# Performance work log

Measured on AMD Instinct MI355X. Metric: run time of the kernel, lower is better.

## Reference

```python
import jax, jax.numpy as jnp
import numpy as np

N = 32768       # tokens
D_IN = 1024     # input_dim
D_OUT = 1024    # output_dim
E = 8           # num_experts
TOP_K = 2


def setup_inputs() -> dict:
    key = jax.random.key(0)
    k1, k2, k3, k4, k5 = jax.random.split(key, 5)
    scale = 1.0 / np.sqrt(D_IN)
    return {
        "x": jax.random.normal(k1, (N, D_IN), dtype=jnp.float32),
        "Wg": jax.random.uniform(k2, (E, D_IN), jnp.float32, -scale, scale),
        "bg": jax.random.uniform(k3, (E,), jnp.float32, -scale, scale),
        "W": jax.random.uniform(k4, (E, D_OUT, D_IN), jnp.float32, -scale, scale),
        "b": jax.random.uniform(k5, (E, D_OUT), jnp.float32, -scale, scale),
    }


def reference(x, Wg, bg, W, b):
    # Gating: softmax over experts, then top-k (weights NOT renormalized,
    # matching the original module).
    gate_scores = x @ Wg.T + bg                      # [N, E]
    gate_probs = jax.nn.softmax(gate_scores, axis=-1)
    topk_w, topk_idx = jax.lax.top_k(gate_probs, TOP_K)  # [N, K]

    # Per-token combine weight for each expert: sum_k w_k * onehot(idx_k)
    combine = (jax.nn.one_hot(topk_idx, E, dtype=x.dtype)
               * topk_w[..., None]).sum(axis=1)      # [N, E]

    # Dense per-expert GEMM + weighted combine (loop over small fixed E).
    out = jnp.zeros((x.shape[0], D_OUT), dtype=x.dtype)
    for e in range(E):
        out = out + combine[:, e:e + 1] * (x @ W[e].T + b[e])
    return out
```

## Files before the change

kernel.cpp:

```cpp
#include <hip/hip_runtime.h>
#include <hip/hip_bf16.h>
#include <cstdint>
#include <cstddef>

#define N_TOK   32768
#define D_IN    1024
#define D_OUT   1024
#define NE      8

#define BM 256
#define BN 256
#define BK 32
#define NTILES (D_IN / BK)

typedef __attribute__((ext_vector_type(4))) float floatx4;
typedef __attribute__((ext_vector_type(8))) short bf16x8;

__device__ __forceinline__ unsigned short f2bf(float f) {
  union { float f; unsigned int u; } v; v.f = f;
  unsigned int u = v.u + 0x7fffu + ((v.u >> 16) & 1u);
  return (unsigned short)(u >> 16);
}

__device__ __forceinline__ unsigned short f2h(float f) {
  union { _Float16 hf; unsigned short us; } c; c.hf = (_Float16)f; return c.us;
}
__device__ __forceinline__ float h2f(unsigned short u) {
  union { _Float16 hf; unsigned short us; } c; c.us = u; return (float)c.hf;
}

__device__ __forceinline__ void gload_lds16(const void* g, void* l) {
  __builtin_amdgcn_global_load_lds(
      (const __attribute__((address_space(1))) unsigned int*)g,
      (__attribute__((address_space(3))) unsigned int*)l, 16, 0, 0);
}

__global__ __launch_bounds__(256) void prep_kernel(
    const float* __restrict__ x,
    const float* __restrict__ Wg,
    const float* __restrict__ bg,
    const float* __restrict__ W,
    unsigned short* __restrict__ xb,
    unsigned short* __restrict__ Wb,
    int* __restrict__ counts,
    int* __restrict__ bids,
    float* __restrict__ bw,
    int* __restrict__ tok2slot,
    float* __restrict__ out,
    int zero_out)
{
  __shared__ float wg_lds[NE * D_IN];
  __shared__ int lcnt[NE];
  __shared__ int basee[NE];
  __shared__ int   tok_e[64][2];
  __shared__ int   tok_s[64][2];
  __shared__ float tok_w[64][2];

  const int blk = blockIdx.x;
  const int tid = threadIdx.x;

  if (blk >= 1024) {
    if (!zero_out) return;
    float4* o4 = (float4*)out;
    const int base = (blk - 1024) * 4096;
#pragma unroll
    for (int i = 0; i < 16; ++i)
      o4[base + i * 256 + tid] = (float4){0.f, 0.f, 0.f, 0.f};
    return;
  }
  if (blk >= 512) {
    const float4* s = (const float4*)W;
    const int base = (blk - 512) * 4096;
#pragma unroll
    for (int i = 0; i < 16; ++i) {
      int idx = base + i * 256 + tid;
      float4 v = s[idx];
      ushort4 h;
      h.x = f2bf(v.x); h.y = f2bf(v.y); h.z = f2bf(v.z); h.w = f2bf(v.w);
      ((ushort4*)Wb)[idx] = h;
    }
    return;
  }

  {
    const float4* s = (const float4*)Wg;
    float4* d = (float4*)wg_lds;
    for (int i = tid; i < NE * D_IN / 4; i += 256) d[i] = s[i];
  }
  if (tid < NE) lcnt[tid] = 0;
  __syncthreads();

  const int wave = tid >> 6, lane = tid & 63;
  const float4* x4 = (const float4*)x;
  const float4* w4 = (const float4*)wg_lds;

  for (int t = 0; t < 16; ++t) {
    const int lt = wave * 16 + t;
    const int n  = blk * 64 + lt;
    float4 xv[4];
    float acc[NE];
#pragma unroll
    for (int e = 0; e < NE; ++e) acc[e] = 0.f;
#pragma unroll
    for (int j = 0; j < 4; ++j) {
      xv[j] = x4[(size_t)n * 256 + j * 64 + lane];
#pragma unroll
      for (int e = 0; e < NE; ++e) {
        float4 w = w4[e * 256 + j * 64 + lane];
        acc[e] += xv[j].x * w.x + xv[j].y * w.y + xv[j].z * w.z + xv[j].w * w.w;
      }
    }
#pragma unroll
    for (int j = 0; j < 4; ++j) {
      ushort4 h;
      h.x = f2bf(xv[j].x); h.y = f2bf(xv[j].y);
      h.z = f2bf(xv[j].z); h.w = f2bf(xv[j].w);
      ((ushort4*)xb)[(size_t)n * 256 + j * 64 + lane] = h;
    }
#pragma unroll
    for (int e = 0; e < NE; ++e)
#pragma unroll
      for (int s = 32; s > 0; s >>= 1)
        acc[e] += __shfl_xor(acc[e], s, 64);

    if (lane == 0) {
      float sc[NE];
#pragma unroll
      for (int e = 0; e < NE; ++e) sc[e] = acc[e] + bg[e];
      float m = sc[0];
#pragma unroll
      for (int e = 1; e < NE; ++e) m = fmaxf(m, sc[e]);
      float p[NE], den = 0.f;
#pragma unroll
      for (int e = 0; e < NE; ++e) { p[e] = __expf(sc[e] - m); den += p[e]; }
      int e1 = 0;
#pragma unroll
      for (int e = 1; e < NE; ++e) if (sc[e] > sc[e1]) e1 = e;
      int e2 = (e1 == 0) ? 1 : 0;
#pragma unroll
      for (int e = 0; e < NE; ++e) if (e != e1 && sc[e] > sc[e2]) e2 = e;
      float inv = 1.f / den;
      tok_e[lt][0] = e1; tok_w[lt][0] = p[e1] * inv; tok_s[lt][0] = atomicAdd(&lcnt[e1], 1);
      tok_e[lt][1] = e2; tok_w[lt][1] = p[e2] * inv; tok_s[lt][1] = atomicAdd(&lcnt[e2], 1);
    }
  }
  __syncthreads();
  if (tid < NE) basee[tid] = atomicAdd(&counts[tid], lcnt[tid]);
  __syncthreads();
  if (tid < 128) {
    int lt = tid >> 1, kk = tid & 1;
    int e = tok_e[lt][kk];
    int slot = basee[e] + tok_s[lt][kk];
    int token = blk * 64 + lt;
    bids[e * N_TOK + slot] = token;
    bw[e * N_TOK + slot]   = tok_w[lt][kk];
    tok2slot[token * 2 + kk] = (e << 15) | slot;
  }
}

__global__ __launch_bounds__(512, 2) void moe_gemm_kernel(
    const unsigned short* __restrict__ xb,
    const unsigned short* __restrict__ Wb,
    const float* __restrict__ bias,
    const int* __restrict__ counts,
    const int* __restrict__ bids,
    const float* __restrict__ bw,
    float* __restrict__ out,
    void* __restrict__ y,
    int mode)
{
  const int bid = blockIdx.x;
  const int e   = bid & 7;
  const int nt  = (bid >> 3) & 3;
  const int mt  = bid >> 5;
  const int cnt = counts[e];
  const int row0 = mt << 8;
  if (row0 >= cnt) return;
  const int rows = min(BM, cnt - row0);

  __shared__ alignas(16) unsigned short Ald[3][BM * BK];
  __shared__ alignas(16) unsigned short Bld[3][BN * BK];
  __shared__ int   ids[BM];
  __shared__ float wts[BM];

  const int tid = threadIdx.x;
  if (tid < BM) {
    int src = (tid < rows) ? tid : 0;
    ids[tid] = bids[e * N_TOK + row0 + src];
    wts[tid] = (tid < rows) ? bw[e * N_TOK + row0 + tid] : 0.f;
  }
  __syncthreads();

  const int w    = tid >> 6;
  const int lane = tid & 63;
  const int wm   = w >> 2;
  const int wn   = w & 3;
  const int m16  = lane & 15;
  const int quad = lane >> 4;

  const unsigned short* wbe = Wb + (size_t)e * D_OUT * D_IN;

  size_t a_goff[2], b_goff[2];
  int ldsgrp[2];
#pragma unroll
  for (int i2 = 0; i2 < 2; ++i2) {
    const int g = w * 2 + i2;
    const int r = g * 16 + (lane >> 2);
    const int c = (lane & 3) ^ ((r >> 1) & 3);
    a_goff[i2] = (size_t)ids[r] * D_IN + c * 8;
    b_goff[i2] = (size_t)(nt * BN + r) * D_IN + c * 8;
    ldsgrp[i2] = g * 512;
  }

  const int swz  = (quad ^ ((m16 >> 1) & 3)) * 8;
  const int roff = m16 * BK + swz;

  floatx4 acc[8][4];
#pragma unroll
  for (int i = 0; i < 8; ++i)
#pragma unroll
    for (int j = 0; j < 4; ++j) acc[i][j] = (floatx4){0.f, 0.f, 0.f, 0.f};

#pragma unroll
  for (int t0 = 0; t0 < 2; ++t0) {
    const int kb = t0 * BK;
#pragma unroll
    for (int i2 = 0; i2 < 2; ++i2) {
      gload_lds16(xb  + a_goff[i2] + kb, &Ald[t0][ldsgrp[i2]]);
      gload_lds16(wbe + b_goff[i2] + kb, &Bld[t0][ldsgrp[i2]]);
    }
  }

  int rcur = 0, rnxt = 2;
  for (int t = 0; t < NTILES; ++t) {
    const int kb2 = (t + 2 < NTILES ? t + 2 : NTILES - 1) * BK;
    gload_lds16(xb + a_goff[0] + kb2, &Ald[rnxt][ldsgrp[0]]);
    gload_lds16(xb + a_goff[1] + kb2, &Ald[rnxt][ldsgrp[1]]);
    asm volatile("s_waitcnt vmcnt(6)" ::: "memory");
    __builtin_amdgcn_s_barrier();
    asm volatile("" ::: "memory");

    bf16x8 bf[4], af[4];
#pragma unroll
    for (int j = 0; j < 4; ++j)
      bf[j] = *(const bf16x8*)&Bld[rcur][(wn * 64 + j * 16) * BK + roff];
#pragma unroll
    for (int i = 0; i < 4; ++i)
      af[i] = *(const bf16x8*)&Ald[rcur][(wm * 128 + i * 16) * BK + roff];
    __builtin_amdgcn_s_setprio(1);
#pragma unroll
    for (int i = 0; i < 4; ++i)
#pragma unroll
      for (int j = 0; j < 4; ++j)
        acc[i][j] = __builtin_amdgcn_mfma_f32_16x16x32_bf16(af[i], bf[j], acc[i][j], 0, 0, 0);
    __builtin_amdgcn_s_setprio(0);

    gload_lds16(wbe + b_goff[0] + kb2, &Bld[rnxt][ldsgrp[0]]);
    gload_lds16(wbe + b_goff[1] + kb2, &Bld[rnxt][ldsgrp[1]]);
#pragma unroll
    for (int i = 0; i < 4; ++i)
      af[i] = *(const bf16x8*)&Ald[rcur][(wm * 128 + 64 + i * 16) * BK + roff];
    __builtin_amdgcn_s_setprio(1);
#pragma unroll
    for (int i = 0; i < 4; ++i)
#pragma unroll
      for (int j = 0; j < 4; ++j)
        acc[i + 4][j] = __builtin_amdgcn_mfma_f32_16x16x32_bf16(af[i], bf[j], acc[i + 4][j], 0, 0, 0);
    __builtin_amdgcn_s_setprio(0);

    asm volatile("" ::: "memory");
    __builtin_amdgcn_s_barrier();
    asm volatile("" ::: "memory");
    rcur = (rcur == 2) ? 0 : rcur + 1;
    rnxt = (rnxt == 2) ? 0 : rnxt + 1;
  }

  float bv[4];
  int col[4];
#pragma unroll
  for (int j = 0; j < 4; ++j) {
    col[j] = nt * BN + wn * 64 + j * 16 + m16;
    bv[j] = bias[e * D_OUT + col[j]];
  }

  int ybase = 0;
  if (mode) {
#pragma unroll
    for (int i = 0; i < NE; ++i) ybase += (i < e) ? counts[i] : 0;
  }

#pragma unroll
  for (int i = 0; i < 8; ++i) {
#pragma unroll
    for (int r = 0; r < 4; ++r) {
      int rl = wm * 128 + i * 16 + quad * 4 + r;
      if (rl < rows) {
        float wgt = wts[rl];
        if (mode == 0) {
          float* orow = out + (size_t)ids[rl] * D_OUT;
#pragma unroll
          for (int j = 0; j < 4; ++j)
            atomicAdd(&orow[col[j]], wgt * (acc[i][j][r] + bv[j]));
        } else if (mode == 2) {
          float* yrow = (float*)y + (size_t)(ybase + row0 + rl) * D_OUT;
#pragma unroll
          for (int j = 0; j < 4; ++j)
            yrow[col[j]] = wgt * (acc[i][j][r] + bv[j]);
        } else {
          unsigned short* yrow = (unsigned short*)y + (size_t)(ybase + row0 + rl) * D_OUT;
#pragma unroll
          for (int j = 0; j < 4; ++j)
            yrow[col[j]] = f2h(wgt * (acc[i][j][r] + bv[j]));
        }
      }
    }
  }
}

__global__ __launch_bounds__(256) void combine_kernel(
    const void* __restrict__ y,
    const int* __restrict__ counts,
    const int* __restrict__ tok2slot,
    float* __restrict__ out,
    int mode)
{
  __shared__ int pre[NE];
  if (threadIdx.x < NE) {
    int s = 0;
    for (int i = 0; i < threadIdx.x; ++i) s += counts[i];
    pre[threadIdx.x] = s;
  }
  __syncthreads();

  const int total = N_TOK * (D_OUT / 4);
  for (int idx = blockIdx.x * 256 + threadIdx.x; idx < total; idx += 2048 * 256) {
    int row = idx >> 8, c4 = idx & 255;
    int v1 = tok2slot[row * 2], v2 = tok2slot[row * 2 + 1];
    long r1 = pre[v1 >> 15] + (v1 & 32767);
    long r2 = pre[v2 >> 15] + (v2 & 32767);
    float4 o;
    if (mode == 2) {
      const float4* y4 = (const float4*)y;
      float4 a = y4[r1 * 256 + c4];
      float4 b = y4[r2 * 256 + c4];
      o.x = a.x + b.x; o.y = a.y + b.y; o.z = a.z + b.z; o.w = a.w + b.w;
    } else {
      const ushort4* y4 = (const ushort4*)y;
      ushort4 a = y4[r1 * 256 + c4];
      ushort4 b = y4[r2 * 256 + c4];
      o.x = h2f(a.x) + h2f(b.x); o.y = h2f(a.y) + h2f(b.y);
      o.z = h2f(a.z) + h2f(b.z); o.w = h2f(a.w) + h2f(b.w);
    }
    ((float4*)out)[idx] = o;
  }
}

extern "C" void kernel_launch(void* const* d_in, const int* in_sizes, int n_in,
                              void* d_out, int out_size, void* d_ws, size_t ws_size,
                              hipStream_t stream) {
  const float* x  = (const float*)d_in[0];
  const float* Wg = (const float*)d_in[1];
  const float* bg = (const float*)d_in[2];
  const float* W  = (const float*)d_in[3];
  const float* b  = (const float*)d_in[4];
  float* out = (float*)d_out;

  char* ws = (char*)d_ws;
  size_t off = 0;
  int*   counts   = (int*)(ws + off);  off += 4096;
  int*   bids     = (int*)(ws + off);  off += (size_t)NE * N_TOK * 4;
  float* bw       = (float*)(ws + off); off += (size_t)NE * N_TOK * 4;
  int*   tok2slot = (int*)(ws + off);  off += (size_t)N_TOK * 2 * 4;
  unsigned short* xb = (unsigned short*)(ws + off); off += (size_t)N_TOK * D_IN * 2;
  unsigned short* Wb = (unsigned short*)(ws + off); off += (size_t)NE * D_IN * D_OUT * 2;
  void* y = (void*)(ws + off);
  const size_t y_rows = 2 * (size_t)N_TOK;
  const size_t need_f32 = off + y_rows * D_OUT * 4;
  const size_t need_f16 = off + y_rows * D_OUT * 2;

  int mode = (ws_size >= need_f32) ? 2 : (ws_size >= need_f16 ? 1 : 0);

  hipMemsetAsync(counts, 0, NE * sizeof(int), stream);
  prep_kernel<<<mode == 0 ? 3072 : 1024, 256, 0, stream>>>(
      x, Wg, bg, W, xb, Wb, counts, bids, bw, tok2slot, out, mode == 0 ? 1 : 0);
  moe_gemm_kernel<<<NE * 4 * (N_TOK / BM), 512, 0, stream>>>(
      xb, Wb, b, counts, bids, bw, out, y, mode);
  if (mode != 0)
    combine_kernel<<<2048, 256, 0, stream>>>(y, counts, tok2slot, out, mode);
}
```

Measured before the change: 567.9 us.

## Shrink MoE GEMM tiles to 128x128x64 with single-buffered LDS and 256 threads

Replaces the 256x256 tile, 512-thread, triple-buffered K=32 pipeline with 128x128 tiles, K=64 steps, 256 threads and a single LDS buffer. Each iteration loads the whole tile, waits for all loads with vmcnt(0), then computes. The aim is more concurrent blocks per CU and better load balance across ragged expert row counts. The cost is that loads and math no longer overlap, global traffic per FLOP roughly doubles, and more blocks are launched.

New measurement: 511.0 us. 10.0% less time.

```diff
diff --git a/kernel.cpp b/kernel.cpp
--- a/kernel.cpp
+++ b/kernel.cpp
@@ -8,10 +8,10 @@
 #define D_OUT   1024
 #define NE      8
 
-#define BM 256
-#define BN 256
-#define BK 32
-#define NTILES (D_IN / BK)
+#define BM 128
+#define BN 128
+#define BK 64
+#define NKT (D_IN / BK)
 
 typedef __attribute__((ext_vector_type(4))) float floatx4;
 typedef __attribute__((ext_vector_type(8))) short bf16x8;
@@ -158,7 +158,7 @@
   }
 }
 
-__global__ __launch_bounds__(512, 2) void moe_gemm_kernel(
+__global__ __launch_bounds__(256, 3) void moe_gemm_kernel(
     const unsigned short* __restrict__ xb,
     const unsigned short* __restrict__ Wb,
     const float* __restrict__ bias,
@@ -171,15 +171,15 @@
 {
   const int bid = blockIdx.x;
   const int e   = bid & 7;
-  const int nt  = (bid >> 3) & 3;
-  const int mt  = bid >> 5;
+  const int nt  = (bid >> 3) & 7;
+  const int mt  = bid >> 6;
   const int cnt = counts[e];
-  const int row0 = mt << 8;
+  const int row0 = mt << 7;
   if (row0 >= cnt) return;
   const int rows = min(BM, cnt - row0);
 
-  __shared__ alignas(16) unsigned short Ald[3][BM * BK];
-  __shared__ alignas(16) unsigned short Bld[3][BN * BK];
+  __shared__ alignas(16) unsigned short Ald[BM * BK];
+  __shared__ alignas(16) unsigned short Bld[BN * BK];
   __shared__ int   ids[BM];
   __shared__ float wts[BM];
 
@@ -193,86 +193,65 @@
 
   const int w    = tid >> 6;
   const int lane = tid & 63;
-  const int wm   = w >> 2;
-  const int wn   = w & 3;
+  const int wm   = w >> 1, wn = w & 1;
   const int m16  = lane & 15;
   const int quad = lane >> 4;
 
   const unsigned short* wbe = Wb + (size_t)e * D_OUT * D_IN;
 
-  size_t a_goff[2], b_goff[2];
-  int ldsgrp[2];
-#pragma unroll
-  for (int i2 = 0; i2 < 2; ++i2) {
-    const int g = w * 2 + i2;
-    const int r = g * 16 + (lane >> 2);
-    const int c = (lane & 3) ^ ((r >> 1) & 3);
-    a_goff[i2] = (size_t)ids[r] * D_IN + c * 8;
-    b_goff[i2] = (size_t)(nt * BN + r) * D_IN + c * 8;
-    ldsgrp[i2] = g * 512;
-  }
-
-  const int swz  = (quad ^ ((m16 >> 1) & 3)) * 8;
-  const int roff = m16 * BK + swz;
-
-  floatx4 acc[8][4];
-#pragma unroll
-  for (int i = 0; i < 8; ++i)
+  int a_off[4], b_off[4];
+  int lds_off[4];
+#pragma unroll
+  for (int l = 0; l < 4; ++l) {
+    const int q = l * 256 + tid;
+    const int r = q >> 3;
+    const int c = (q & 7) ^ (r & 7);
+    a_off[l] = ids[r] * D_IN + c * 8;
+    b_off[l] = (nt * BN + r) * D_IN + c * 8;
+    lds_off[l] = (l * 256 + w * 64) * 8;
+  }
+
+  floatx4 acc[4][4];
+#pragma unroll
+  for (int i = 0; i < 4; ++i)
 #pragma unroll
     for (int j = 0; j < 4; ++j) acc[i][j] = (floatx4){0.f, 0.f, 0.f, 0.f};
 
-#pragma unroll
-  for (int t0 = 0; t0 < 2; ++t0) {
-    const int kb = t0 * BK;
-#pragma unroll
-    for (int i2 = 0; i2 < 2; ++i2) {
-      gload_lds16(xb  + a_goff[i2] + kb, &Ald[t0][ldsgrp[i2]]);
-      gload_lds16(wbe + b_goff[i2] + kb, &Bld[t0][ldsgrp[i2]]);
-    }
-  }
-
-  int rcur = 0, rnxt = 2;
-  for (int t = 0; t < NTILES; ++t) {
-    const int kb2 = (t + 2 < NTILES ? t + 2 : NTILES - 1) * BK;
-    gload_lds16(xb + a_goff[0] + kb2, &Ald[rnxt][ldsgrp[0]]);
-    gload_lds16(xb + a_goff[1] + kb2, &Ald[rnxt][ldsgrp[1]]);
-    asm volatile("s_waitcnt vmcnt(6)" ::: "memory");
+  for (int kt = 0; kt < NKT; ++kt) {
+    const int kb = kt * BK;
+#pragma unroll
+    for (int l = 0; l < 4; ++l)
+      gload_lds16(xb + a_off[l] + kb, &Ald[lds_off[l]]);
+#pragma unroll
+    for (int l = 0; l < 4; ++l)
+      gload_lds16(wbe + b_off[l] + kb, &Bld[lds_off[l]]);
+
+    asm volatile("s_waitcnt vmcnt(0)" ::: "memory");
     __builtin_amdgcn_s_barrier();
     asm volatile("" ::: "memory");
 
-    bf16x8 bf[4], af[4];
-#pragma unroll
-    for (int j = 0; j < 4; ++j)
-      bf[j] = *(const bf16x8*)&Bld[rcur][(wn * 64 + j * 16) * BK + roff];
-#pragma unroll
-    for (int i = 0; i < 4; ++i)
-      af[i] = *(const bf16x8*)&Ald[rcur][(wm * 128 + i * 16) * BK + roff];
-    __builtin_amdgcn_s_setprio(1);
-#pragma unroll
-    for (int i = 0; i < 4; ++i)
+#pragma unroll
+    for (int ks = 0; ks < 2; ++ks) {
+      const int sw = (((ks << 2) | quad) ^ (m16 & 7)) * 8;
+      bf16x8 af[4], bf[4];
 #pragma unroll
       for (int j = 0; j < 4; ++j)
-        acc[i][j] = __builtin_amdgcn_mfma_f32_16x16x32_bf16(af[i], bf[j], acc[i][j], 0, 0, 0);
-    __builtin_amdgcn_s_setprio(0);
-
-    gload_lds16(wbe + b_goff[0] + kb2, &Bld[rnxt][ldsgrp[0]]);
-    gload_lds16(wbe + b_goff[1] + kb2, &Bld[rnxt][ldsgrp[1]]);
-#pragma unroll
-    for (int i = 0; i < 4; ++i)
-      af[i] = *(const bf16x8*)&Ald[rcur][(wm * 128 + 64 + i * 16) * BK + roff];
-    __builtin_amdgcn_s_setprio(1);
-#pragma unroll
-    for (int i = 0; i < 4; ++i)
-#pragma unroll
-      for (int j = 0; j < 4; ++j)
-        acc[i + 4][j] = __builtin_amdgcn_mfma_f32_16x16x32_bf16(af[i], bf[j], acc[i + 4][j], 0, 0, 0);
-    __builtin_amdgcn_s_setprio(0);
+        bf[j] = *(const bf16x8*)&Bld[(wn * 64 + j * 16 + m16) * BK + sw];
+#pragma unroll
+      for (int i = 0; i < 4; ++i)
+        af[i] = *(const bf16x8*)&Ald[(wm * 64 + i * 16 + m16) * BK + sw];
+      __builtin_amdgcn_s_setprio(1);
+#pragma unroll
+      for (int i = 0; i < 4; ++i)
+#pragma unroll
+        for (int j = 0; j < 4; ++j)
+          acc[i][j] = __builtin_amdgcn_mfma_f32_16x16x32_bf16(af[i], bf[j], acc[i][j], 0, 0, 0);
+      __builtin_amdgcn_s_setprio(0);
+    }
 
     asm volatile("" ::: "memory");
     __builtin_amdgcn_s_barrier();
     asm volatile("" ::: "memory");
-    rcur = (rcur == 2) ? 0 : rcur + 1;
-    rnxt = (rnxt == 2) ? 0 : rnxt + 1;
   }
 
   float bv[4];
@@ -290,10 +269,10 @@
   }
 
 #pragma unroll
-  for (int i = 0; i < 8; ++i) {
+  for (int i = 0; i < 4; ++i) {
 #pragma unroll
     for (int r = 0; r < 4; ++r) {
-      int rl = wm * 128 + i * 16 + quad * 4 + r;
+      int rl = wm * 64 + i * 16 + quad * 4 + r;
       if (rl < rows) {
         float wgt = wts[rl];
         if (mode == 0) {
@@ -383,7 +362,7 @@
   hipMemsetAsync(counts, 0, NE * sizeof(int), stream);
   prep_kernel<<<mode == 0 ? 3072 : 1024, 256, 0, stream>>>(
       x, Wg, bg, W, xb, Wb, counts, bids, bw, tok2slot, out, mode == 0 ? 1 : 0);
-  moe_gemm_kernel<<<NE * 4 * (N_TOK / BM), 512, 0, stream>>>(
+  moe_gemm_kernel<<<NE * 8 * (N_TOK / BM), 256, 0, stream>>>(
       xb, Wb, b, counts, bids, bw, out, y, mode);
   if (mode != 0)
     combine_kernel<<<2048, 256, 0, stream>>>(y, counts, tok2slot, out, mode);
```
